# Kernel optimization log

Measured on AMD Instinct MI355X. Metric: run time of the kernel, lower is better.

## Reference

```python
import jax, jax.numpy as jnp
import numpy as np

ELT_BATCH = 64            # number of candidate elements (rows)
OBS_PER_ELT = 100_000     # observations per element (uniform row_lengths)
DATA_SIZE = ELT_BATCH * OBS_PER_ELT
THRESH_DEG = 2.0
THRESH_HIT_PROB_POST = 0.95


def _deg2dist(deg):
    # chord length on unit sphere subtended by angle `deg`
    return 2.0 * np.sin(np.radians(deg) / 2.0)


def setup_inputs() -> dict:
    key = jax.random.key(0)
    k1, k2, k3, k4 = jax.random.split(key, 4)
    # observed unit directions
    u_obs = jax.random.normal(k1, (DATA_SIZE, 3), dtype=jnp.float32)
    u_obs = u_obs / jnp.linalg.norm(u_obs, axis=-1, keepdims=True)
    # predicted directions = observed + small perturbation so a realistic
    # fraction of observations fall inside the 2-degree threshold
    noise = 0.01 * jax.random.normal(k2, (DATA_SIZE, 3), dtype=jnp.float32)
    u_pred = u_obs + noise
    u_pred = u_pred / jnp.linalg.norm(u_pred, axis=-1, keepdims=True)
    # mixture-model params per element: hit fraction h in (0.1, 0.9), decay lam in (1, 10)
    h = 0.1 + 0.8 * jax.random.uniform(k3, (ELT_BATCH,), dtype=jnp.float32)
    lam = 1.0 + 9.0 * jax.random.uniform(k4, (ELT_BATCH,), dtype=jnp.float32)
    # squared chord-distance threshold per element (constant buffer in the layer)
    thresh_s2 = jnp.full((ELT_BATCH,), np.float32(_deg2dist(THRESH_DEG) ** 2), dtype=jnp.float32)
    return {"u_pred": u_pred, "u_obs": u_obs, "h": h, "lam": lam, "thresh_s2": thresh_s2}


def reference(u_pred, u_obs, h, lam, thresh_s2):
    B = thresh_s2.shape[0]
    n_per = u_pred.shape[0] // B  # uniform row_lengths
    seg_ids = jnp.repeat(jnp.arange(B, dtype=jnp.int32), n_per)  # [data_size]

    # squared chord distance per observation
    du = u_pred - u_obs                                # [N, 3]
    s2 = jnp.sum(jnp.square(du), axis=-1)              # [N]

    thresh_rep = jnp.repeat(thresh_s2, n_per)          # [N]
    h_rep = jnp.repeat(h, n_per)                       # [N]
    lam_rep = jnp.repeat(lam, n_per)                   # [N]

    is_close = s2 < thresh_rep                         # [N] bool
    v = s2 / thresh_rep                                # normalized squared distance in [0,1) where close

    # truncated-exponential mixture model
    emlx = jnp.exp(-lam_rep * v)
    p_hit_cond = emlx * lam_rep / (1.0 - jnp.exp(-lam_rep))
    p_hit = h_rep * p_hit_cond
    p = p_hit + (1.0 - h_rep)

    # mask instead of boolean_mask: excluded entries contribute 0 to segment sums
    log_p = jnp.where(is_close, jnp.log(p), 0.0)
    p_hit_post = p_hit / p
    is_real_hit = p_hit_post > THRESH_HIT_PROB_POST
    p_hit_filtered = jnp.where(is_close & is_real_hit, p_hit_post, 0.0)

    log_like = jax.ops.segment_sum(log_p, seg_ids, num_segments=B)        # [B]
    hits = jax.ops.segment_sum(p_hit_filtered, seg_ids, num_segments=B)   # [B]
    hits_raw = hits  # original code sums p_hit_filtered for both outputs
    return (log_like, hits, hits_raw)
```

## Files before the change

kernel.cpp:

```cpp
#include <hip/hip_runtime.h>


constexpr int ELT_BATCH       = 64;
constexpr int OBS_PER_ELT     = 100000;
constexpr int F4_PER_SEG      = OBS_PER_ELT * 3 / 4;
constexpr int CHUNK_F4        = 63;
constexpr int CHUNKS_PER_SEG  = (F4_PER_SEG + CHUNK_F4 - 1) / CHUNK_F4;
constexpr int BLOCKS_PER_SEG  = 32;
constexpr int BLOCK           = 256;
constexpr int WAVES_PER_BLOCK = BLOCK / 64;
constexpr int WAVES_PER_SEG   = BLOCKS_PER_SEG * WAVES_PER_BLOCK;
constexpr int PAIR_STRIDE     = 2 * WAVES_PER_SEG;
constexpr int ITERS           = 5;

__device__ __forceinline__ float wave_reduce_sum(float v) {
    #pragma unroll
    for (int off = 32; off > 0; off >>= 1)
        v += __shfl_down(v, off, 64);
    return v;
}

__device__ __forceinline__ void eval_chunk(
    const float4 a, const float4 b, const int act,
    const int lane, const bool m0, const bool m1,
    const float nli, const float coef, const float omh, const float th,
    float& ll, float& hs)
{
    const float d0 = a.x - b.x, d1 = a.y - b.y, d2 = a.z - b.z, d3 = a.w - b.w;
    const float q0 = d0 * d0, q1 = d1 * d1, q2 = d2 * d2, q3 = d3 * d3;

    const float head = m1 ? (q0 + q1) : q0;
    const float hn   = __shfl_down(head, 1, 64);

    const float t12 = q1 + q2;
    const float s2A = m0 ? (q0 + t12) : (m1 ? (q2 + q3 + hn) : (t12 + q3));
    const float s2B = q3 + hn;

    const bool lv = lane < act;
    {
        const float e  = __expf(nli * s2A);
        const float ph = coef * e;
        const float p  = ph + omh;
        const float lp = __logf(p);
        const float po = ph / p;
        const bool  cl = (s2A < th) && lv;
        ll += cl ? lp : 0.0f;
        hs += (cl && po > 0.95f) ? po : 0.0f;
    }
    {
        const float e  = __expf(nli * s2B);
        const float ph = coef * e;
        const float p  = ph + omh;
        const float lp = __logf(p);
        const float po = ph / p;
        const bool  cl = (s2B < th) && lv && m0;
        ll += cl ? lp : 0.0f;
        hs += (cl && po > 0.95f) ? po : 0.0f;
    }
}

__global__ __launch_bounds__(BLOCK, 8) void TrajectoryScore_58145267253396_kernel(
    const float4* __restrict__ pred4,
    const float4* __restrict__ obs4,
    const float*  __restrict__ h_arr,
    const float*  __restrict__ lam_arr,
    const float*  __restrict__ th_arr,
    float*        __restrict__ out)
{
    const int seg        = blockIdx.x / BLOCKS_PER_SEG;
    const int blk_in_seg = blockIdx.x % BLOCKS_PER_SEG;
    const int tid  = threadIdx.x;
    const int lane = tid & 63;
    const int wave = tid >> 6;
    const int wseg = blk_in_seg * WAVES_PER_BLOCK + wave;

    const float h      = h_arr[seg];
    const float lam    = lam_arr[seg];
    const float th     = th_arr[seg];
    const float inv_th = 1.0f / th;
    const float coef   = h * lam / (1.0f - __expf(-lam));
    const float omh    = 1.0f - h;
    const float nli    = -lam * inv_th;

    const int  m  = lane % 3;
    const bool m0 = (m == 0);
    const bool m1 = (m == 1);

    const int seg_f4 = seg * F4_PER_SEG;

    float ll = 0.0f;
    float hs = 0.0f;

    auto ld = [&](int c, float4& A, float4& B) {
        const int idx = seg_f4 + min(c * CHUNK_F4 + lane, F4_PER_SEG - 1);
        A = pred4[idx];
        B = obs4[idx];
    };

    float4 A0, B0, A1, B1, A0n, B0n, A1n, B1n;
    ld(wseg,                   A0, B0);
    ld(wseg + WAVES_PER_SEG,   A1, B1);

    #pragma unroll
    for (int it = 0; it < ITERS; ++it) {
        const int cn = wseg + (it + 1) * PAIR_STRIDE;
        ld(cn,                 A0n, B0n);
        ld(cn + WAVES_PER_SEG, A1n, B1n);
        __builtin_amdgcn_sched_barrier(0);

        const int c = wseg + it * PAIR_STRIDE;
        eval_chunk(A0, B0, F4_PER_SEG - c * CHUNK_F4 < CHUNK_F4 ? F4_PER_SEG - c * CHUNK_F4 : CHUNK_F4,
                   lane, m0, m1, nli, coef, omh, th, ll, hs);
        eval_chunk(A1, B1, F4_PER_SEG - (c + WAVES_PER_SEG) * CHUNK_F4 < CHUNK_F4
                              ? F4_PER_SEG - (c + WAVES_PER_SEG) * CHUNK_F4 : CHUNK_F4,
                   lane, m0, m1, nli, coef, omh, th, ll, hs);

        A0 = A0n; B0 = B0n; A1 = A1n; B1 = B1n;
    }

    ll = wave_reduce_sum(ll);
    hs = wave_reduce_sum(hs);

    __shared__ float sll[WAVES_PER_BLOCK];
    __shared__ float shs[WAVES_PER_BLOCK];
    if (lane == 0) { sll[wave] = ll; shs[wave] = hs; }
    __syncthreads();
    if (tid == 0) {
        float L = 0.0f, H = 0.0f;
        #pragma unroll
        for (int w = 0; w < WAVES_PER_BLOCK; ++w) { L += sll[w]; H += shs[w]; }
        atomicAdd(&out[seg], L);
        atomicAdd(&out[ELT_BATCH + seg], H);
        atomicAdd(&out[2 * ELT_BATCH + seg], H);
    }
}

extern "C" void kernel_launch(void* const* d_in, const int* in_sizes, int n_in,
                              void* d_out, int out_size, void* d_ws, size_t ws_size,
                              hipStream_t stream) {
    const float4* pred4   = (const float4*)d_in[0];
    const float4* obs4    = (const float4*)d_in[1];
    const float*  h_arr   = (const float*)d_in[2];
    const float*  lam_arr = (const float*)d_in[3];
    const float*  th_arr  = (const float*)d_in[4];
    float* out = (float*)d_out;

    hipMemsetAsync(out, 0, out_size * sizeof(float), stream);

    dim3 grid(ELT_BATCH * BLOCKS_PER_SEG);
    dim3 block(BLOCK);
    TrajectoryScore_58145267253396_kernel<<<grid, block, 0, stream>>>(
        pred4, obs4, h_arr, lam_arr, th_arr, out);
}
```

Baseline: 179.1 us.

## Stream input chunks through LDS with async global_load_lds double buffering

Replaces register-held prefetch of float4 pairs with direct global-to-LDS async loads into two per-wave slots, then reads each chunk back from LDS before computing. The loop becomes a runtime loop over the wave's chunks, with explicit vmcnt and lgkmcnt waits. The aim is to keep more loads in flight with fewer VGPRs. The cost is extra LDS traffic and serialising waits. The loop also issues loads past the last needed chunk, which are clamped by the index min.

Result: no change. 180.1 us (+0.6%).

```diff
diff --git a/kernel.cpp b/kernel.cpp
--- a/kernel.cpp
+++ b/kernel.cpp
@@ -10,8 +10,10 @@
 constexpr int BLOCK           = 256;
 constexpr int WAVES_PER_BLOCK = BLOCK / 64;
 constexpr int WAVES_PER_SEG   = BLOCKS_PER_SEG * WAVES_PER_BLOCK;
-constexpr int PAIR_STRIDE     = 2 * WAVES_PER_SEG;
-constexpr int ITERS           = 5;
+constexpr int NSLOT           = 2;
+
+typedef const __attribute__((address_space(1))) void g_void;
+typedef __attribute__((address_space(3))) void l_void;
 
 __device__ __forceinline__ float wave_reduce_sum(float v) {
     #pragma unroll
@@ -67,6 +69,9 @@
     const float*  __restrict__ th_arr,
     float*        __restrict__ out)
 {
+    __shared__ float4 sp[WAVES_PER_BLOCK][NSLOT][64];
+    __shared__ float4 so[WAVES_PER_BLOCK][NSLOT][64];
+
     const int seg        = blockIdx.x / BLOCKS_PER_SEG;
     const int blk_in_seg = blockIdx.x % BLOCKS_PER_SEG;
     const int tid  = threadIdx.x;
@@ -88,34 +93,39 @@
 
     const int seg_f4 = seg * F4_PER_SEG;
 
+    const int NJ = (CHUNKS_PER_SEG - 1 - wseg) / WAVES_PER_SEG + 1;
+
+    auto stage = [&](int j, int slot) {
+        const int c   = wseg + j * WAVES_PER_SEG;
+        const int idx = seg_f4 + min(c * CHUNK_F4 + lane, F4_PER_SEG - 1);
+        __builtin_amdgcn_global_load_lds((g_void*)(pred4 + idx),
+                                         (l_void*)(&sp[wave][slot][0]), 16, 0, 0);
+        __builtin_amdgcn_global_load_lds((g_void*)(obs4 + idx),
+                                         (l_void*)(&so[wave][slot][0]), 16, 0, 0);
+    };
+
+    stage(0, 0);
+    stage(1, 1);
+
     float ll = 0.0f;
     float hs = 0.0f;
 
-    auto ld = [&](int c, float4& A, float4& B) {
-        const int idx = seg_f4 + min(c * CHUNK_F4 + lane, F4_PER_SEG - 1);
-        A = pred4[idx];
-        B = obs4[idx];
-    };
+    for (int j = 0; j < NJ; ++j) {
+        const int slot = j & 1;
 
-    float4 A0, B0, A1, B1, A0n, B0n, A1n, B1n;
-    ld(wseg,                   A0, B0);
-    ld(wseg + WAVES_PER_SEG,   A1, B1);
+        asm volatile("s_waitcnt vmcnt(2)" ::: "memory");
 
-    #pragma unroll
-    for (int it = 0; it < ITERS; ++it) {
-        const int cn = wseg + (it + 1) * PAIR_STRIDE;
-        ld(cn,                 A0n, B0n);
-        ld(cn + WAVES_PER_SEG, A1n, B1n);
+        const float4 a = sp[wave][slot][lane];
+        const float4 b = so[wave][slot][lane];
+
+        asm volatile("s_waitcnt lgkmcnt(0)" ::: "memory");
         __builtin_amdgcn_sched_barrier(0);
 
-        const int c = wseg + it * PAIR_STRIDE;
-        eval_chunk(A0, B0, F4_PER_SEG - c * CHUNK_F4 < CHUNK_F4 ? F4_PER_SEG - c * CHUNK_F4 : CHUNK_F4,
-                   lane, m0, m1, nli, coef, omh, th, ll, hs);
-        eval_chunk(A1, B1, F4_PER_SEG - (c + WAVES_PER_SEG) * CHUNK_F4 < CHUNK_F4
-                              ? F4_PER_SEG - (c + WAVES_PER_SEG) * CHUNK_F4 : CHUNK_F4,
-                   lane, m0, m1, nli, coef, omh, th, ll, hs);
+        stage(j + 2, slot);
 
-        A0 = A0n; B0 = B0n; A1 = A1n; B1 = B1n;
+        const int c   = wseg + j * WAVES_PER_SEG;
+        const int act = min(CHUNK_F4, F4_PER_SEG - c * CHUNK_F4);
+        eval_chunk(a, b, act, lane, m0, m1, nli, coef, omh, th, ll, hs);
     }
 
     ll = wave_reduce_sum(ll);
```

## Assign contiguous chunk ranges per wave and batch loads in groups of four

Applied to the files above, without the earlier changes.

Each wave now processes a contiguous run of 9 or 10 chunks instead of chunks strided across the segment. Loads are issued in groups of four before evaluating, replacing the double-buffered prefetch loop and its sched_barrier. The occupancy hint in launch_bounds is dropped so the compiler can use more registers for the deeper load batches. Contiguous per-wave access may improve DRAM locality but changes how concurrent waves spread across memory.

Result: no change. 177.5 us (-0.9%).

```diff
diff --git a/kernel.cpp b/kernel.cpp
--- a/kernel.cpp
+++ b/kernel.cpp
@@ -5,13 +5,11 @@
 constexpr int OBS_PER_ELT     = 100000;
 constexpr int F4_PER_SEG      = OBS_PER_ELT * 3 / 4;
 constexpr int CHUNK_F4        = 63;
-constexpr int CHUNKS_PER_SEG  = (F4_PER_SEG + CHUNK_F4 - 1) / CHUNK_F4;
+constexpr int LAST_CHUNK      = 1190;
 constexpr int BLOCKS_PER_SEG  = 32;
 constexpr int BLOCK           = 256;
 constexpr int WAVES_PER_BLOCK = BLOCK / 64;
-constexpr int WAVES_PER_SEG   = BLOCKS_PER_SEG * WAVES_PER_BLOCK;
-constexpr int PAIR_STRIDE     = 2 * WAVES_PER_SEG;
-constexpr int ITERS           = 5;
+constexpr int SPLIT_W         = 39;
 
 __device__ __forceinline__ float wave_reduce_sum(float v) {
     #pragma unroll
@@ -59,7 +57,7 @@
     }
 }
 
-__global__ __launch_bounds__(BLOCK, 8) void TrajectoryScore_58145267253396_kernel(
+__global__ __launch_bounds__(BLOCK) void TrajectoryScore_58145267253396_kernel(
     const float4* __restrict__ pred4,
     const float4* __restrict__ obs4,
     const float*  __restrict__ h_arr,
@@ -73,6 +71,9 @@
     const int lane = tid & 63;
     const int wave = tid >> 6;
     const int wseg = blk_in_seg * WAVES_PER_BLOCK + wave;
+
+    const int cw = (wseg < SPLIT_W) ? wseg * 10 : SPLIT_W * 10 + (wseg - SPLIT_W) * 9;
+    const int NJ = (wseg < SPLIT_W) ? 10 : 9;
 
     const float h      = h_arr[seg];
     const float lam    = lam_arr[seg];
@@ -88,34 +89,35 @@
 
     const int seg_f4 = seg * F4_PER_SEG;
 
+    auto addr = [&](int j) {
+        const int c = min(cw + j, LAST_CHUNK);
+        return seg_f4 + min(c * CHUNK_F4 + lane, F4_PER_SEG - 1);
+    };
+    auto actf = [&](int j) {
+        return (j < NJ) ? min(CHUNK_F4, F4_PER_SEG - (cw + j) * CHUNK_F4) : 0;
+    };
+
     float ll = 0.0f;
     float hs = 0.0f;
 
-    auto ld = [&](int c, float4& A, float4& B) {
-        const int idx = seg_f4 + min(c * CHUNK_F4 + lane, F4_PER_SEG - 1);
-        A = pred4[idx];
-        B = obs4[idx];
+    auto group4 = [&](int j0) {
+        const int i0 = addr(j0), i1 = addr(j0 + 1), i2 = addr(j0 + 2), i3 = addr(j0 + 3);
+        const float4 a0 = pred4[i0], a1 = pred4[i1], a2 = pred4[i2], a3 = pred4[i3];
+        const float4 b0 = obs4[i0],  b1 = obs4[i1],  b2 = obs4[i2],  b3 = obs4[i3];
+        eval_chunk(a0, b0, actf(j0),     lane, m0, m1, nli, coef, omh, th, ll, hs);
+        eval_chunk(a1, b1, actf(j0 + 1), lane, m0, m1, nli, coef, omh, th, ll, hs);
+        eval_chunk(a2, b2, actf(j0 + 2), lane, m0, m1, nli, coef, omh, th, ll, hs);
+        eval_chunk(a3, b3, actf(j0 + 3), lane, m0, m1, nli, coef, omh, th, ll, hs);
     };
 
-    float4 A0, B0, A1, B1, A0n, B0n, A1n, B1n;
-    ld(wseg,                   A0, B0);
-    ld(wseg + WAVES_PER_SEG,   A1, B1);
-
-    #pragma unroll
-    for (int it = 0; it < ITERS; ++it) {
-        const int cn = wseg + (it + 1) * PAIR_STRIDE;
-        ld(cn,                 A0n, B0n);
-        ld(cn + WAVES_PER_SEG, A1n, B1n);
-        __builtin_amdgcn_sched_barrier(0);
-
-        const int c = wseg + it * PAIR_STRIDE;
-        eval_chunk(A0, B0, F4_PER_SEG - c * CHUNK_F4 < CHUNK_F4 ? F4_PER_SEG - c * CHUNK_F4 : CHUNK_F4,
-                   lane, m0, m1, nli, coef, omh, th, ll, hs);
-        eval_chunk(A1, B1, F4_PER_SEG - (c + WAVES_PER_SEG) * CHUNK_F4 < CHUNK_F4
-                              ? F4_PER_SEG - (c + WAVES_PER_SEG) * CHUNK_F4 : CHUNK_F4,
-                   lane, m0, m1, nli, coef, omh, th, ll, hs);
-
-        A0 = A0n; B0 = B0n; A1 = A1n; B1 = B1n;
+    group4(0);
+    group4(4);
+    {
+        const int i0 = addr(8), i1 = addr(9);
+        const float4 a0 = pred4[i0], a1 = pred4[i1];
+        const float4 b0 = obs4[i0],  b1 = obs4[i1];
+        eval_chunk(a0, b0, actf(8), lane, m0, m1, nli, coef, omh, th, ll, hs);
+        eval_chunk(a1, b1, actf(9), lane, m0, m1, nli, coef, omh, th, ll, hs);
     }
 
     ll = wave_reduce_sum(ll);
```
